# Kernel optimization log

Hardware: AMD Instinct MI355X
Metric: run time of the kernel (lower is better)

The kernel has to match this reference:

```python
import jax, jax.numpy as jnp
import numpy as np

TOP_K = 8          # n_activated_experts
ROUTE_SCALE = 2.5  # route_scale


def setup_inputs() -> dict:
    key = jax.random.key(0)
    k1, k2, k3 = jax.random.split(key, 3)
    T, D, E = 16384, 7168, 256
    x = jax.random.normal(k1, (T, D), dtype=jnp.float32)
    # nn.Linear weight layout: [out_features, in_features]
    W = jax.random.normal(k2, (E, D), dtype=jnp.float32) * (1.0 / np.sqrt(D))
    bias = jax.random.normal(k3, (E,), dtype=jnp.float32) * 0.01
    return {"x": x, "W": W, "bias": bias}


def reference(x, W, bias):
    # logits: [T, E] = x [T, D] @ W.T [D, E]
    logits = jnp.einsum("td,ed->te", x, W)
    scores = jax.nn.sigmoid(logits)              # original_scores
    biased = scores + bias                       # bias only affects expert selection
    _, indices = jax.lax.top_k(biased, TOP_K)    # [T, K] int32
    weights = jnp.take_along_axis(scores, indices, axis=-1)  # gather unbiased scores
    weights = weights / jnp.sum(weights, axis=-1, keepdims=True)  # sigmoid renorm
    weights = weights * ROUTE_SCALE
    return weights.astype(x.dtype), indices
```

## Files before the change

### kernel.cpp

```cpp
#include <hip/hip_runtime.h>
#include <cmath>

namespace {

typedef _Float16 half8 __attribute__((ext_vector_type(8)));
typedef float f32x4 __attribute__((ext_vector_type(4)));

constexpr int kTokens = 16384;
constexpr int kD      = 7168;
constexpr int kE      = 256;
constexpr int kTopK   = 8;
constexpr float kRouteScale = 2.5f;

constexpr int BM     = 32;
constexpr int BK     = 32;
constexpr int KSTEP  = 128;
constexpr int NT     = kD / BK;
constexpr int NSTEP  = kD / KSTEP;
constexpr float kS  = 4096.0f;
constexpr float kC  = 0.000244140625f;
constexpr size_t kWsTileB = 32768;
constexpr size_t kWsNeed  = (size_t)NT * kWsTileB;

__global__ void wconv_kernel(const float* __restrict__ W, unsigned char* __restrict__ ws)
{
    const int e = blockIdx.x;
    const int t = threadIdx.x;
    const float* src = W + (size_t)e * kD + (size_t)t * 8;
    float v[8];
    *reinterpret_cast<float4*>(v)     = *reinterpret_cast<const float4*>(src);
    *reinterpret_cast<float4*>(v + 4) = *reinterpret_cast<const float4*>(src + 4);
    half8 h, l;
#pragma unroll
    for (int j = 0; j < 8; ++j) {
        _Float16 hh = (_Float16)v[j];
        h[j] = hh;
        l[j] = (_Float16)((v[j] - (float)hh) * kS);
    }
    const int kt = t >> 2;
    const int kg = t & 3;
    const size_t off = (size_t)kt * kWsTileB +
                       (size_t)(((e >> 4) << 6) + (kg << 4) + (e & 15)) * 16;
    *reinterpret_cast<half8*>(ws + off)         = h;
    *reinterpret_cast<half8*>(ws + off + 16384) = l;
}

__global__ __launch_bounds__(512, 4)
void gate_mfma(const float* __restrict__ x,
               const unsigned char* __restrict__ wst,
               const float* __restrict__ bias,
               float* __restrict__ out)
{
    __shared__ unsigned char lds[32896];

    const int t    = threadIdx.x;
    const int lane = t & 63;
    const int wid  = t >> 6;
    const int m0   = blockIdx.x * BM;
    const int l15  = lane & 15;
    const int lg   = lane >> 4;

    const int srow = t >> 4;
    const int skc  = t & 15;
    const unsigned waddr = (unsigned)(((skc >> 2) << 12) + ((srow >> 4) << 10) +
                                      ((skc & 3) << 8) + ((((srow & 15) ^ skc) & 15) << 4));
    const float* xsrc = x + (size_t)(m0 + srow) * kD + (size_t)(skc * 8);

    unsigned roff[4];
#pragma unroll
    for (int kk = 0; kk < 4; ++kk)
        roff[kk] = (unsigned)((kk << 12) + (lg << 8) +
                              (((l15 ^ ((kk << 2) + lg)) & 15) << 4));

    const unsigned char* wb = wst + (size_t)(wid * 2) * 1024 + (size_t)lane * 16;

    f32x4 acc0[2][2], acc1[2][2], accL[2][2], cmpL[2][2];
#pragma unroll
    for (int i = 0; i < 2; ++i)
#pragma unroll
        for (int j = 0; j < 2; ++j) {
            acc0[i][j] = f32x4{0.f,0.f,0.f,0.f};
            acc1[i][j] = f32x4{0.f,0.f,0.f,0.f};
            accL[i][j] = f32x4{0.f,0.f,0.f,0.f};
            cmpL[i][j] = f32x4{0.f,0.f,0.f,0.f};
        }

    half8 breg[2][2][2];

    auto LOADB = [&](int pp, int kt) {
        const unsigned char* p = wb + (size_t)kt * kWsTileB;
#pragma unroll
        for (int j = 0; j < 2; ++j) {
            breg[pp][j][0] = *reinterpret_cast<const half8*>(p + j * 1024);
            breg[pp][j][1] = *reinterpret_cast<const half8*>(p + j * 1024 + 16384);
        }
    };
    auto WRITESTEP = [&](unsigned base, const float4& a, const float4& b) {
        float v[8];
        *reinterpret_cast<float4*>(v)     = a;
        *reinterpret_cast<float4*>(v + 4) = b;
        half8 h0, h1;
#pragma unroll
        for (int j = 0; j < 8; ++j) {
            const _Float16 hh = (_Float16)v[j];
            h0[j] = hh;
            h1[j] = (_Float16)((v[j] - (float)hh) * kS);
        }
        *reinterpret_cast<half8*>(&lds[base + waddr])        = h0;
        *reinterpret_cast<half8*>(&lds[base + waddr + 2048]) = h1;
    };

    {
        float4 a = *reinterpret_cast<const float4*>(xsrc);
        float4 b = *reinterpret_cast<const float4*>(xsrc + 4);
        LOADB(0, 0);
        WRITESTEP(0, a, b);
    }
    __syncthreads();

    for (int s = 0; s < NSTEP; ++s) {
        const unsigned bufc = (unsigned)((s & 1) << 14);
        const unsigned bufn = (unsigned)(((s + 1) & 1) << 14);
        const bool pre = (s + 1 < NSTEP);
        float4 nv0{0,0,0,0}, nv1{0,0,0,0};
        if (pre) {
            const float* p = xsrc + (s + 1) * KSTEP;
            nv0 = *reinterpret_cast<const float4*>(p);
            nv1 = *reinterpret_cast<const float4*>(p + 4);
        }

#pragma unroll
        for (int kk = 0; kk < 4; ++kk) {
            const int kt = s * 4 + kk;
            if (kt + 1 < NT) LOADB((kk + 1) & 1, kt + 1);
            half8 xh[2], xm[2];
#pragma unroll
            for (int i = 0; i < 2; ++i) {
                xh[i] = *reinterpret_cast<const half8*>(&lds[bufc + roff[kk] + i * 1024]);
                xm[i] = *reinterpret_cast<const half8*>(&lds[bufc + roff[kk] + i * 1024 + 2048]);
            }
#pragma unroll
            for (int i = 0; i < 2; ++i)
#pragma unroll
                for (int j = 0; j < 2; ++j)
                    acc0[i][j] = __builtin_amdgcn_mfma_f32_16x16x32_f16(xh[i], breg[kk & 1][j][0], acc0[i][j], 0, 0, 0);
#pragma unroll
            for (int i = 0; i < 2; ++i)
#pragma unroll
                for (int j = 0; j < 2; ++j)
                    acc1[i][j] = __builtin_amdgcn_mfma_f32_16x16x32_f16(xm[i], breg[kk & 1][j][0], acc1[i][j], 0, 0, 0);
#pragma unroll
            for (int i = 0; i < 2; ++i)
#pragma unroll
                for (int j = 0; j < 2; ++j)
                    acc1[i][j] = __builtin_amdgcn_mfma_f32_16x16x32_f16(xh[i], breg[kk & 1][j][1], acc1[i][j], 0, 0, 0);
        }

        if (pre) WRITESTEP(bufn, nv0, nv1);

        if (((s + 1) & 3) == 0) {
#pragma unroll
            for (int i = 0; i < 2; ++i)
#pragma unroll
                for (int j = 0; j < 2; ++j) {
                    f32x4 y = acc0[i][j] - cmpL[i][j];
                    f32x4 ss = accL[i][j] + y;
                    cmpL[i][j] = (ss - accL[i][j]) - y;
                    accL[i][j] = ss;
                    acc0[i][j] = f32x4{0.f,0.f,0.f,0.f};
                }
        }
        __syncthreads();
    }

    float (*sc)[257] = reinterpret_cast<float (*)[257]>(lds);
#pragma unroll
    for (int j = 0; j < 2; ++j) {
        const int col  = wid * 32 + j * 16 + l15;
        const float bv = bias[col];
#pragma unroll
        for (int i = 0; i < 2; ++i) {
            f32x4 z = (accL[i][j] + acc0[i][j]) + kC * acc1[i][j];
#pragma unroll
            for (int r = 0; r < 4; ++r) {
                const int row = i * 16 + lg * 4 + r;
                const float s = 1.0f / (1.0f + expf(-z[r]));
                sc[row][col] = s + bv;
            }
        }
    }
    __syncthreads();

    const int rr = t >> 4;
    const int g  = t & 15;

    float cval[kTopK];
    int   cidx[kTopK];

#pragma unroll
    for (int r = 0; r < kTopK; ++r) {
        float best = -INFINITY;
        int   bi   = kE;
        const float* rowp = sc[rr] + g * 16;
#pragma unroll 8
        for (int c = 0; c < 16; ++c) {
            const float v  = rowp[c];
            const int   ci = g * 16 + c;
            if (v > best || (v == best && ci < bi)) { best = v; bi = ci; }
        }
#pragma unroll
        for (int off = 8; off > 0; off >>= 1) {
            const float ov = __shfl_xor(best, off, 16);
            const int   oi = __shfl_xor(bi,   off, 16);
            if (ov > best || (ov == best && oi < bi)) { best = ov; bi = oi; }
        }
        cval[r] = best;
        cidx[r] = bi;
        if ((bi >> 4) == g) sc[rr][bi] = -INFINITY;
        __syncthreads();
    }

    if (g == 0) {
        float uw[kTopK];
        float wsum = 0.0f;
#pragma unroll
        for (int r = 0; r < kTopK; ++r) {
            uw[r] = cval[r] - bias[cidx[r]];
            wsum += uw[r];
        }
        const float scale = kRouteScale / wsum;
        const size_t grow = (size_t)(m0 + rr);
#pragma unroll
        for (int r = 0; r < kTopK; ++r)
            out[grow * kTopK + r] = uw[r] * scale;
#pragma unroll
        for (int r = 0; r < kTopK; ++r)
            out[(size_t)kTokens * kTopK + grow * kTopK + r] = (float)cidx[r];
    }
}

constexpr int FBM = 32;
constexpr int FBK = 32;
constexpr int XS_STRIDE = 36;
constexpr int SC_STRIDE = 260;

__global__ __launch_bounds__(256, 2)
void gate_fused(const float* __restrict__ x,
                const float* __restrict__ W,
                const float* __restrict__ bias,
                float* __restrict__ out)
{
    __shared__ float smem[FBK * XS_STRIDE + FBK * kE];
    float (*xs)[XS_STRIDE] = reinterpret_cast<float (*)[XS_STRIDE]>(smem);
    float (*ws)[kE]        = reinterpret_cast<float (*)[kE]>(smem + FBK * XS_STRIDE);
    float (*sc)[SC_STRIDE] = reinterpret_cast<float (*)[SC_STRIDE]>(smem);

    const int t  = threadIdx.x;
    const int tx = t & 31;
    const int ty = t >> 5;
    const int m0 = blockIdx.x * FBM;
    const int lm = t >> 3;
    const int lc = t & 7;

    float acc[4][8];
    float cmp[4][8];
#pragma unroll
    for (int i = 0; i < 4; ++i)
#pragma unroll
        for (int j = 0; j < 8; ++j) { acc[i][j] = 0.0f; cmp[i][j] = 0.0f; }

    const float* xrow = x + (size_t)(m0 + lm) * kD;
    const float* wrow = W + (size_t)t * kD;

    for (int k0 = 0; k0 < kD; k0 += FBK) {
        float4 xv = *reinterpret_cast<const float4*>(xrow + k0 + 4 * lc);
        float4 wv[8];
#pragma unroll
        for (int i = 0; i < 8; ++i)
            wv[i] = *reinterpret_cast<const float4*>(wrow + k0 + 4 * i);
        __syncthreads();
        xs[4 * lc + 0][lm] = xv.x; xs[4 * lc + 1][lm] = xv.y;
        xs[4 * lc + 2][lm] = xv.z; xs[4 * lc + 3][lm] = xv.w;
#pragma unroll
        for (int i = 0; i < 8; ++i) {
            ws[4 * i + 0][t] = wv[i].x; ws[4 * i + 1][t] = wv[i].y;
            ws[4 * i + 2][t] = wv[i].z; ws[4 * i + 3][t] = wv[i].w;
        }
        __syncthreads();
        float p[4][8];
#pragma unroll
        for (int i = 0; i < 4; ++i)
#pragma unroll
            for (int j = 0; j < 8; ++j) p[i][j] = 0.0f;
#pragma unroll
        for (int k = 0; k < FBK; ++k) {
            float a[4], b[8];
            *reinterpret_cast<float4*>(a)     = *reinterpret_cast<const float4*>(&xs[k][4 * ty]);
            *reinterpret_cast<float4*>(b)     = *reinterpret_cast<const float4*>(&ws[k][4 * tx]);
            *reinterpret_cast<float4*>(b + 4) = *reinterpret_cast<const float4*>(&ws[k][128 + 4 * tx]);
#pragma unroll
            for (int i = 0; i < 4; ++i)
#pragma unroll
                for (int j = 0; j < 8; ++j)
                    p[i][j] = fmaf(a[i], b[j], p[i][j]);
        }
#pragma unroll
        for (int i = 0; i < 4; ++i)
#pragma unroll
            for (int j = 0; j < 8; ++j) {
                const float y = p[i][j] - cmp[i][j];
                const float s = acc[i][j] + y;
                cmp[i][j] = (s - acc[i][j]) - y;
                acc[i][j] = s;
            }
    }
    __syncthreads();
#pragma unroll
    for (int i = 0; i < 4; ++i) {
        const int row = 4 * ty + i;
#pragma unroll
        for (int j = 0; j < 8; ++j) {
            const int col = (j < 4) ? (4 * tx + j) : (128 + 4 * tx + (j - 4));
            const float s = 1.0f / (1.0f + expf(-acc[i][j]));
            sc[row][col] = s + bias[col];
        }
    }
    __syncthreads();
    const int rr = t >> 3;
    const int g  = t & 7;
    float cval[kTopK];
    int   cidx[kTopK];
#pragma unroll
    for (int r = 0; r < kTopK; ++r) {
        float best = -INFINITY;
        int   bi   = kE;
        const float* rowp = sc[rr] + g * 32;
#pragma unroll 8
        for (int c = 0; c < 32; ++c) {
            const float v  = rowp[c];
            const int   ci = g * 32 + c;
            if (v > best || (v == best && ci < bi)) { best = v; bi = ci; }
        }
#pragma unroll
        for (int off = 4; off > 0; off >>= 1) {
            const float ov = __shfl_xor(best, off, 8);
            const int   oi = __shfl_xor(bi,   off, 8);
            if (ov > best || (ov == best && oi < bi)) { best = ov; bi = oi; }
        }
        cval[r] = best; cidx[r] = bi;
        if ((bi >> 5) == g) sc[rr][bi] = -INFINITY;
        __syncthreads();
    }
    if (g == 0) {
        float uw[kTopK];
        float wsum = 0.0f;
#pragma unroll
        for (int r = 0; r < kTopK; ++r) { uw[r] = cval[r] - bias[cidx[r]]; wsum += uw[r]; }
        const float scale = kRouteScale / wsum;
        const size_t grow = (size_t)(m0 + rr);
#pragma unroll
        for (int r = 0; r < kTopK; ++r) out[grow * kTopK + r] = uw[r] * scale;
#pragma unroll
        for (int r = 0; r < kTopK; ++r)
            out[(size_t)kTokens * kTopK + grow * kTopK + r] = (float)cidx[r];
    }
}

}

extern "C" void kernel_launch(void* const* d_in, const int* in_sizes, int n_in,
                              void* d_out, int out_size, void* d_ws, size_t ws_size,
                              hipStream_t stream)
{
    const float* x    = (const float*)d_in[0];
    const float* W    = (const float*)d_in[1];
    const float* bias = (const float*)d_in[2];
    float* out = (float*)d_out;

    if (ws_size >= kWsNeed) {
        unsigned char* ws = (unsigned char*)d_ws;
        hipLaunchKernelGGL(wconv_kernel, dim3(kE), dim3(kD / 8), 0, stream, W, ws);
        hipLaunchKernelGGL(gate_mfma, dim3(kTokens / BM), dim3(512), 0, stream, x, ws, bias, out);
    } else {
        hipLaunchKernelGGL(gate_fused, dim3(kTokens / FBM), dim3(256), 0, stream, x, W, bias, out);
    }
}
```

Baseline: 259.7 us.

## Software-pipeline LDS A-fragment loads and split W hi/lo register prefetch

Restructures the inner MFMA loop so the x fragments for the next k-subtile are read from LDS while the current MFMAs run, and the W high part is double-buffered while the W low-correction part is loaded just in time, which cuts live registers. It replaces the Kahan compensated flush with plain summation every 8 steps instead of 4, and removes a __syncthreads inside the top-k selection loop. Dropping that barrier risks a race on the shared score row between the -inf write and the next round's reads, and the plain summation can lose precision in near-tie top-k choices.

```diff
diff --git a/kernel.cpp b/kernel.cpp
--- a/kernel.cpp
+++ b/kernel.cpp
@@ -66,15 +66,9 @@
                                       ((skc & 3) << 8) + ((((srow & 15) ^ skc) & 15) << 4));
     const float* xsrc = x + (size_t)(m0 + srow) * kD + (size_t)(skc * 8);
 
-    unsigned roff[4];
-#pragma unroll
-    for (int kk = 0; kk < 4; ++kk)
-        roff[kk] = (unsigned)((kk << 12) + (lg << 8) +
-                              (((l15 ^ ((kk << 2) + lg)) & 15) << 4));
-
     const unsigned char* wb = wst + (size_t)(wid * 2) * 1024 + (size_t)lane * 16;
 
-    f32x4 acc0[2][2], acc1[2][2], accL[2][2], cmpL[2][2];
+    f32x4 acc0[2][2], acc1[2][2], accL[2][2];
 #pragma unroll
     for (int i = 0; i < 2; ++i)
 #pragma unroll
@@ -82,18 +76,30 @@
             acc0[i][j] = f32x4{0.f,0.f,0.f,0.f};
             acc1[i][j] = f32x4{0.f,0.f,0.f,0.f};
             accL[i][j] = f32x4{0.f,0.f,0.f,0.f};
-            cmpL[i][j] = f32x4{0.f,0.f,0.f,0.f};
-        }
-
-    half8 breg[2][2][2];
-
-    auto LOADB = [&](int pp, int kt) {
+        }
+
+    half8 bh[2][2];
+    half8 bl[2];
+    half8 axh[2][2];
+    half8 axm[2][2];
+
+    auto LOADBH = [&](int pp, int kt) {
         const unsigned char* p = wb + (size_t)kt * kWsTileB;
-#pragma unroll
-        for (int j = 0; j < 2; ++j) {
-            breg[pp][j][0] = *reinterpret_cast<const half8*>(p + j * 1024);
-            breg[pp][j][1] = *reinterpret_cast<const half8*>(p + j * 1024 + 16384);
-        }
+        bh[pp][0] = *reinterpret_cast<const half8*>(p);
+        bh[pp][1] = *reinterpret_cast<const half8*>(p + 1024);
+    };
+    auto LOADBL = [&](int kt) {
+        const unsigned char* p = wb + (size_t)kt * kWsTileB + 16384;
+        bl[0] = *reinterpret_cast<const half8*>(p);
+        bl[1] = *reinterpret_cast<const half8*>(p + 1024);
+    };
+    auto LDA = [&](int pp, unsigned bufc, int kk) {
+        const unsigned base = bufc + (unsigned)(kk << 12) + (unsigned)(lg << 8) +
+                              (unsigned)((((l15 ^ ((kk << 2) + lg)) & 15) << 4));
+        axh[pp][0] = *reinterpret_cast<const half8*>(&lds[base]);
+        axh[pp][1] = *reinterpret_cast<const half8*>(&lds[base + 1024]);
+        axm[pp][0] = *reinterpret_cast<const half8*>(&lds[base + 2048]);
+        axm[pp][1] = *reinterpret_cast<const half8*>(&lds[base + 3072]);
     };
     auto WRITESTEP = [&](unsigned base, const float4& a, const float4& b) {
         float v[8];
@@ -113,7 +119,7 @@
     {
         float4 a = *reinterpret_cast<const float4*>(xsrc);
         float4 b = *reinterpret_cast<const float4*>(xsrc + 4);
-        LOADB(0, 0);
+        LOADBH(0, 0);
         WRITESTEP(0, a, b);
     }
     __syncthreads();
@@ -122,6 +128,8 @@
         const unsigned bufc = (unsigned)((s & 1) << 14);
         const unsigned bufn = (unsigned)(((s + 1) & 1) << 14);
         const bool pre = (s + 1 < NSTEP);
+
+        LDA(0, bufc, 0);
         float4 nv0{0,0,0,0}, nv1{0,0,0,0};
         if (pre) {
             const float* p = xsrc + (s + 1) * KSTEP;
@@ -132,41 +140,35 @@
 #pragma unroll
         for (int kk = 0; kk < 4; ++kk) {
             const int kt = s * 4 + kk;
-            if (kt + 1 < NT) LOADB((kk + 1) & 1, kt + 1);
-            half8 xh[2], xm[2];
-#pragma unroll
-            for (int i = 0; i < 2; ++i) {
-                xh[i] = *reinterpret_cast<const half8*>(&lds[bufc + roff[kk] + i * 1024]);
-                xm[i] = *reinterpret_cast<const half8*>(&lds[bufc + roff[kk] + i * 1024 + 2048]);
-            }
+            LOADBL(kt);
+            if (kk < 3) LDA((kk + 1) & 1, bufc, kk + 1);
+            if (kt + 1 < NT) LOADBH((kk + 1) & 1, kt + 1);
+            const int pp = kk & 1;
 #pragma unroll
             for (int i = 0; i < 2; ++i)
 #pragma unroll
                 for (int j = 0; j < 2; ++j)
-                    acc0[i][j] = __builtin_amdgcn_mfma_f32_16x16x32_f16(xh[i], breg[kk & 1][j][0], acc0[i][j], 0, 0, 0);
+                    acc0[i][j] = __builtin_amdgcn_mfma_f32_16x16x32_f16(axh[pp][i], bh[pp][j], acc0[i][j], 0, 0, 0);
 #pragma unroll
             for (int i = 0; i < 2; ++i)
 #pragma unroll
                 for (int j = 0; j < 2; ++j)
-                    acc1[i][j] = __builtin_amdgcn_mfma_f32_16x16x32_f16(xm[i], breg[kk & 1][j][0], acc1[i][j], 0, 0, 0);
+                    acc1[i][j] = __builtin_amdgcn_mfma_f32_16x16x32_f16(axm[pp][i], bh[pp][j], acc1[i][j], 0, 0, 0);
 #pragma unroll
             for (int i = 0; i < 2; ++i)
 #pragma unroll
                 for (int j = 0; j < 2; ++j)
-                    acc1[i][j] = __builtin_amdgcn_mfma_f32_16x16x32_f16(xh[i], breg[kk & 1][j][1], acc1[i][j], 0, 0, 0);
+                    acc1[i][j] = __builtin_amdgcn_mfma_f32_16x16x32_f16(axh[pp][i], bl[j], acc1[i][j], 0, 0, 0);
         }
 
         if (pre) WRITESTEP(bufn, nv0, nv1);
 
-        if (((s + 1) & 3) == 0) {
+        if (((s + 1) & 7) == 0) {
 #pragma unroll
             for (int i = 0; i < 2; ++i)
 #pragma unroll
                 for (int j = 0; j < 2; ++j) {
-                    f32x4 y = acc0[i][j] - cmpL[i][j];
-                    f32x4 ss = accL[i][j] + y;
-                    cmpL[i][j] = (ss - accL[i][j]) - y;
-                    accL[i][j] = ss;
+                    accL[i][j] += acc0[i][j];
                     acc0[i][j] = f32x4{0.f,0.f,0.f,0.f};
                 }
         }
@@ -217,7 +219,6 @@
         cval[r] = best;
         cidx[r] = bi;
         if ((bi >> 4) == g) sc[rr][bi] = -INFINITY;
-        __syncthreads();
     }
 
     if (g == 0) {
```

Result: no change. 256.6 us (-1.2%).
